# Performance work log

Measured on AMD Instinct MI355X. Metric: run time of the kernel, lower is better.

## Reference

```python
import jax, jax.numpy as jnp
import numpy as np

B, C, H, W = 8, 112, 64, 64
O, K, G = 112, 3, 14
STRIDE, PAD = 1, 1
K2 = K * K


def setup_inputs() -> dict:
    key = jax.random.key(0)
    ks = jax.random.split(key, 5)
    return {
        "x": jax.random.normal(ks[0], (B, C, H, W), jnp.float32),
        # offset/mask generator conv (3x3, stride 1, pad 1) -> 3*G*K2 channels
        "pg_weight": jax.random.normal(ks[1], (3 * G * K2, C, 3, 3), jnp.float32) * 0.01,
        "pg_bias": jax.random.normal(ks[2], (3 * G * K2,), jnp.float32) * 0.01,
        # main deformable-conv weight [O, C/groups, K, K] (groups=1) and bias
        "weight": jax.random.normal(ks[3], (O, C, K, K), jnp.float32) * 0.05,
        "bias": jax.random.normal(ks[4], (O,), jnp.float32) * 0.01,
    }


def _bilinear_sample(img, y, x):
    # img: [Cg, H, W]; y, x: [K2, Ho, Wo] float sampling coords.
    # Out-of-bounds corners contribute zero (torchvision semantics).
    Hi, Wi = img.shape[1], img.shape[2]
    y0 = jnp.floor(y)
    x0 = jnp.floor(x)

    def corner(yy, xx):
        valid = (yy >= 0) & (yy <= Hi - 1) & (xx >= 0) & (xx <= Wi - 1)
        yc = jnp.clip(yy, 0, Hi - 1).astype(jnp.int32)
        xc = jnp.clip(xx, 0, Wi - 1).astype(jnp.int32)
        v = img[:, yc, xc]  # [Cg, K2, Ho, Wo]
        return jnp.where(valid[None], v, jnp.zeros((), img.dtype))

    wy1 = (y - y0)[None]
    wx1 = (x - x0)[None]
    wy0 = 1.0 - wy1
    wx0 = 1.0 - wx1
    return (corner(y0, x0) * wy0 * wx0
            + corner(y0, x0 + 1) * wy0 * wx1
            + corner(y0 + 1, x0) * wy1 * wx0
            + corner(y0 + 1, x0 + 1) * wy1 * wx1)


def reference(x, pg_weight, pg_bias, weight, bias):
    Bn, Cn, Hn, Wn = x.shape
    Ho = (Hn + 2 * PAD - K) // STRIDE + 1
    Wo = (Wn + 2 * PAD - K) // STRIDE + 1
    # param_generator: 3x3 conv, stride 1, pad 1
    pg = jax.lax.conv_general_dilated(
        x, pg_weight, (1, 1), ((1, 1), (1, 1)),
        dimension_numbers=("NCHW", "OIHW", "NCHW"))
    pg = pg + pg_bias[None, :, None, None]
    GK2 = G * K2
    oh, ow, m = pg[:, :GK2], pg[:, GK2:2 * GK2], pg[:, 2 * GK2:]
    # module concatenates [oh, ow]; deform_conv2d interprets channels as [G, K2, (dy, dx)]
    off = jnp.concatenate([oh, ow], axis=1).reshape(Bn, G, K2, 2, Ho, Wo)
    dy, dx = off[:, :, :, 0], off[:, :, :, 1]
    mask = jax.nn.sigmoid(m).reshape(Bn, G, K2, Ho, Wo)
    # base sampling grid per kernel tap (row-major K*K order)
    ky = (jnp.arange(K2) // K).astype(x.dtype)
    kx = (jnp.arange(K2) % K).astype(x.dtype)
    py = (jnp.arange(Ho, dtype=x.dtype) * STRIDE - PAD)[None, :, None] + ky[:, None, None]
    px = (jnp.arange(Wo, dtype=x.dtype) * STRIDE - PAD)[None, None, :] + kx[:, None, None]
    ys = py[None, None] + dy  # [B, G, K2, Ho, Wo]
    xs = px[None, None] + dx
    xg = x.reshape(Bn, G, Cn // G, Hn, Wn)
    # vmap over batch, then offset group
    sampled = jax.vmap(jax.vmap(_bilinear_sample))(xg, ys, xs)  # [B, G, Cg, K2, Ho, Wo]
    sampled = sampled * mask[:, :, None]
    sampled = sampled.reshape(Bn, Cn, K2, Ho, Wo)
    out = jnp.einsum("bckhw,ock->bohw", sampled, weight.reshape(weight.shape[0], Cn, K2))
    return out + bias[None, :, None, None]
```

## Files before the change

kernel.cpp:

```cpp
#include <hip/hip_runtime.h>
#include <math.h>

#define Bn 8
#define Cn 112
#define Hn 64
#define Wn 64
#define On 112
#define Gn 14
#define PGC 378
#define HW 4096
#define CKW 1008
#define KP 1024
#define NP 384
#define XROW 4356
#define PG_MT 137
#define MPAD (PG_MT * 256)
#define PLANE_ROWS 34848
#define XGUARD 67
#define XTG_ROWS_TOTAL 558080

typedef __attribute__((ext_vector_type(8))) short bf16x8;
typedef __attribute__((ext_vector_type(4))) float f32x4;

__device__ __forceinline__ unsigned short f2bf(float f) {
    union { float f; unsigned int u; } v; v.f = f;
    unsigned int r = v.u + 0x7fffu + ((v.u >> 16) & 1u);
    return (unsigned short)(r >> 16);
}
__device__ __forceinline__ float bf2f(unsigned short u) {
    union { unsigned int u; float f; } v; v.u = ((unsigned int)u) << 16;
    return v.f;
}
__device__ __forceinline__ float bflo(unsigned int u) {
    union { unsigned int u; float f; } v; v.u = u << 16; return v.f;
}
__device__ __forceinline__ float bfhi(unsigned int u) {
    union { unsigned int u; float f; } v; v.u = u & 0xffff0000u; return v.f;
}
__device__ __forceinline__ void gload_lds16(const void* g, void* l) {
    __builtin_amdgcn_global_load_lds(
        (const __attribute__((address_space(1))) unsigned int*)g,
        (__attribute__((address_space(3))) unsigned int*)l, 16, 0, 0);
}

#define ZN XTG_ROWS_TOTAL
#define B2N (NP * KP)
#define WBN (128 * KP)
__global__ __launch_bounds__(256) void prep_kernel(
    const float* __restrict__ pgw, const float* __restrict__ w,
    unsigned short* __restrict__ XTGa, unsigned short* __restrict__ B2,
    unsigned short* __restrict__ WB)
{
    int t = blockIdx.x * 256 + threadIdx.x;
    if (t < ZN) {
        const uint4 z = {0, 0, 0, 0};
        reinterpret_cast<uint4*>(XTGa)[t] = z;
        return;
    }
    t -= ZN;
    if (t < B2N) {
        int oc = t >> 10, ck = t & 1023;
        int pg_ = ck >> 3, cc = ck & 7;
        int tap = pg_ / 14, pl = pg_ % 14;
        float v = (pg_ < 126 && oc < PGC)
            ? pgw[(size_t)oc * CKW + (pl * 8 + cc) * 9 + tap] : 0.f;
        B2[t] = f2bf(v);
        return;
    }
    t -= B2N;
    if (t < WBN) {
        int oc = t >> 10, ck = t & 1023;
        float v = 0.f;
        if (oc < On && ck < CKW) {
            int g = ck / 72, r = ck % 72;
            int k = r >> 3, cc = r & 7;
            v = w[(size_t)oc * CKW + (g * 8 + cc) * 9 + k];
        }
        WB[t] = f2bf(v);
    }
}

__global__ __launch_bounds__(256) void xpose_kernel(
    const float* __restrict__ x, unsigned short* __restrict__ XTG)
{
    __shared__ unsigned short lds[64][136];

    const int tid = threadIdx.x;
    const int y = blockIdx.x, b = blockIdx.y;
    const int xx = tid & 63, cw = tid >> 6;

    const float* xb = x + (size_t)b * Cn * HW + y * 64;
    #pragma unroll
    for (int p = 0; p < 28; ++p) {
        int c = p * 4 + cw;
        lds[xx][c] = f2bf(xb[(size_t)c * HW + xx]);
    }
    __syncthreads();

    #pragma unroll
    for (int q = 0; q < 4; ++q) {
        int task = q * 256 + tid;
        if (task < 896) {
            int g = task >> 6;
            int x2 = task & 63;
            unsigned short* dst = XTG + ((size_t)g * PLANE_ROWS
                + (size_t)b * XROW + (y + 1) * 66 + x2 + 1) * 8;
            *reinterpret_cast<uint4*>(dst) =
                *reinterpret_cast<const uint4*>(&lds[x2][g * 8]);
        }
    }
}

#define A_BUF_B 16384
#define B_BUF_B 8192
__global__ __launch_bounds__(512, 4) void pg_shift_kernel(
    const unsigned short* __restrict__ XTG, const unsigned short* __restrict__ B2,
    const float* __restrict__ pgb, unsigned short* __restrict__ pgBF)
{
    __shared__ __align__(16) unsigned char smem[3 * (A_BUF_B + B_BUF_B)];

    const int tid  = threadIdx.x;
    const int lane = tid & 63;
    const int w    = tid >> 6;
    const int wr   = w >> 1;
    const int wc   = w & 1;
    const int m0   = blockIdx.x * 256;
    const int n0   = blockIdx.y * 128;
    const int fr   = lane & 15, fq = lane >> 4;

    f32x4 acc[4][4] = {};

    auto Abuf = [&](int b) -> unsigned char* { return smem + b * A_BUF_B; };
    auto Bbuf = [&](int b) -> unsigned char* {
        return smem + 3 * A_BUF_B + b * B_BUF_B; };

    auto stage = [&](int buf, int kt) {
        #pragma unroll
        for (int s = 0; s < 2; ++s) {
            int r = w * 32 + s * 16 + (lane >> 2);
            int ch = (lane & 3) ^ ((r >> 1) & 3);
            int pg_ = kt * 4 + ch;
            int tap = pg_ / 14, pl = pg_ % 14;
            int shift = (tap / 3 - 1) * 66 + (tap % 3) - 1;
            if (pg_ >= 126) { pl = 14; shift = 0; }
            gload_lds16(XTG + ((long)pl * PLANE_ROWS + (long)(m0 + r) + shift) * 8,
                        Abuf(buf) + (w * 32 + s * 16) * 64);
        }
        {
            int r = w * 16 + (lane >> 2);
            int ch = (lane & 3) ^ ((r >> 1) & 3);
            gload_lds16(&B2[(size_t)(n0 + r) * KP + kt * 32 + ch * 8],
                        Bbuf(buf) + (w * 16) * 64);
        }
    };

    stage(0, 0);
    stage(1, 1);

    for (int kt = 0; kt < 32; ++kt) {
        if (kt < 31) asm volatile("s_waitcnt vmcnt(3)" ::: "memory");
        else         asm volatile("s_waitcnt vmcnt(0)" ::: "memory");
        __builtin_amdgcn_s_barrier();
        asm volatile("" ::: "memory");

        const int cur = kt % 3;
        const unsigned char* Ab = Abuf(cur);
        const unsigned char* Bb = Bbuf(cur);

        bf16x8 a[4], b[4];
        #pragma unroll
        for (int mi = 0; mi < 4; ++mi) {
            int r = wr * 64 + mi * 16 + fr;
            a[mi] = *reinterpret_cast<const bf16x8*>(
                Ab + r * 64 + ((fq ^ ((r >> 1) & 3)) << 4));
        }
        #pragma unroll
        for (int ni = 0; ni < 4; ++ni) {
            int r = wc * 64 + ni * 16 + fr;
            b[ni] = *reinterpret_cast<const bf16x8*>(
                Bb + r * 64 + ((fq ^ ((r >> 1) & 3)) << 4));
        }
        if (kt + 2 < 32) stage((kt + 2) % 3, kt + 2);

        __builtin_amdgcn_s_setprio(1);
        #pragma unroll
        for (int mi = 0; mi < 4; ++mi)
            #pragma unroll
            for (int ni = 0; ni < 4; ++ni)
                acc[mi][ni] = __builtin_amdgcn_mfma_f32_16x16x32_bf16(
                    a[mi], b[ni], acc[mi][ni], 0, 0, 0);
        __builtin_amdgcn_s_setprio(0);
    }

    __builtin_amdgcn_s_barrier();
    unsigned short* T = (unsigned short*)smem;

    #pragma unroll
    for (int ni = 0; ni < 4; ++ni) {
        int ocl = wc * 64 + ni * 16 + fr;
        float bv = (n0 + ocl < PGC) ? pgb[n0 + ocl] : 0.f;
        #pragma unroll
        for (int mi = 0; mi < 4; ++mi) {
            int pxl = wr * 64 + mi * 16 + fq * 4;
            ushort4 pk;
            pk.x = f2bf(acc[mi][ni][0] + bv);
            pk.y = f2bf(acc[mi][ni][1] + bv);
            pk.z = f2bf(acc[mi][ni][2] + bv);
            pk.w = f2bf(acc[mi][ni][3] + bv);
            *reinterpret_cast<ushort4*>(&T[ocl * 264 + pxl]) = pk;
        }
    }
    __builtin_amdgcn_s_barrier();

    const int pxls = tid & 255;
    const int half = tid >> 8;
    const int pxd  = m0 + pxls;
    const int bb   = pxd / XROW;
    const int rem  = pxd - bb * XROW;
    const int yy   = rem / 66 - 1;
    const int xx   = rem - (yy + 1) * 66 - 1;
    const bool valid = (pxd < Bn * XROW) &&
                       ((unsigned)yy < 64u) && ((unsigned)xx < 64u);
    unsigned short* pbase = pgBF + (size_t)bb * PGC * HW + yy * 64 + xx;

    #pragma unroll 4
    for (int oc = 0; oc < 64; ++oc) {
        int ocg = n0 + half * 64 + oc;
        if (ocg >= PGC) break;
        unsigned short v = T[(half * 64 + oc) * 264 + pxls];
        if (valid) pbase[(size_t)ocg * HW] = v;
    }
}

__global__ __launch_bounds__(512, 4) void fused_kernel(
    const unsigned short* __restrict__ XTG, const unsigned short* __restrict__ pg,
    const unsigned short* __restrict__ WB, const float* __restrict__ bias,
    float* __restrict__ out)
{
    __shared__ __align__(16) unsigned char Ab[2][64 * 128];
    __shared__ __align__(16) unsigned char Bb[2][128 * 128];

    const int tid  = threadIdx.x;
    const int lane = tid & 63;
    const int w    = tid >> 6;
    const int fr   = lane & 15, fq = lane >> 4;
    const int mh   = w >> 2;
    const int nq   = w & 3;

    const int bid = (int)blockIdx.x;
    const int blk = (bid & 7) * 64 + (bid >> 3);
    const int px0 = blk * 64;
    const int b   = px0 >> 12;
    const int hw0 = px0 & 4095;

    const int spx = lane;
    const int q   = w;
    const int hw  = hw0 + spx;
    const int sy  = hw >> 6, sx = hw & 63;

    const unsigned short* pgb = pg + (size_t)b * PGC * HW + hw;

    f32x4 acc[2][2] = {};

    unsigned short rdy, rdx, rmv;
    float fdy, fdx, fmv;
    uint4 q00, q01, q10, q11;
    float w00, w01, w10, w11;

    auto issue_pg = [&](int kt) {
        int gk = kt * 8 + q;
        int gkc = min(gk, 125);
        int g = gkc / 9, k = gkc - 9 * g;
        rdy = pgb[(size_t)(18 * g + 2 * k) * HW];
        rdx = pgb[(size_t)(18 * g + 2 * k + 1) * HW];
        rmv = pgb[(size_t)(252 + 9 * g + k) * HW];
    };

    auto issue_gather = [&](int kt1) {
        int gk = kt1 * 8 + q;
        bool valid = gk < 126;
        int gkc = min(gk, 125);
        int g = gkc / 9, k = gkc - 9 * g;
        const int ky = k / 3, kx = k - 3 * ky;
        float m = valid ? 1.f / (1.f + __expf(-fmv)) : 0.f;
        float yf = (float)(sy + ky - 1) + fdy;
        float xf = (float)(sx + kx - 1) + fdx;
        float y0 = floorf(yf), x0 = floorf(xf);
        float wy1 = yf - y0, wx1 = xf - x0;
        float wy0 = 1.f - wy1, wx0 = 1.f - wx1;
        int iy0 = (int)y0, ix0 = (int)x0;
        bool vy0 = (iy0 >= 0) && (iy0 < Hn);
        bool vy1 = (iy0 >= -1) && (iy0 < Hn - 1);
        bool vx0 = (ix0 >= 0) && (ix0 < Wn);
        bool vx1 = (ix0 >= -1) && (ix0 < Wn - 1);
        int cy0 = min(max(iy0, 0), Hn - 1), cy1 = min(max(iy0 + 1, 0), Hn - 1);
        int cx0 = min(max(ix0, 0), Wn - 1), cx1 = min(max(ix0 + 1, 0), Wn - 1);
        w00 = (vy0 && vx0) ? wy0 * wx0 * m : 0.f;
        w01 = (vy0 && vx1) ? wy0 * wx1 * m : 0.f;
        w10 = (vy1 && vx0) ? wy1 * wx0 * m : 0.f;
        w11 = (vy1 && vx1) ? wy1 * wx1 * m : 0.f;
        const unsigned short* xg = XTG +
            ((size_t)g * PLANE_ROWS + (size_t)b * XROW) * 8;
        q00 = *reinterpret_cast<const uint4*>(xg + (size_t)((cy0 + 1) * 66 + cx0 + 1) * 8);
        q01 = *reinterpret_cast<const uint4*>(xg + (size_t)((cy0 + 1) * 66 + cx1 + 1) * 8);
        q10 = *reinterpret_cast<const uint4*>(xg + (size_t)((cy1 + 1) * 66 + cx0 + 1) * 8);
        q11 = *reinterpret_cast<const uint4*>(xg + (size_t)((cy1 + 1) * 66 + cx1 + 1) * 8);
    };

    auto combine_write = [&](int buf) {
        unsigned int c00[4] = {q00.x, q00.y, q00.z, q00.w};
        unsigned int c01[4] = {q01.x, q01.y, q01.z, q01.w};
        unsigned int c10[4] = {q10.x, q10.y, q10.z, q10.w};
        unsigned int c11[4] = {q11.x, q11.y, q11.z, q11.w};
        unsigned int pk[4];
        #pragma unroll
        for (int j = 0; j < 4; ++j) {
            float lo = bflo(c00[j]) * w00 + bflo(c01[j]) * w01 +
                       bflo(c10[j]) * w10 + bflo(c11[j]) * w11;
            float hi = bfhi(c00[j]) * w00 + bfhi(c01[j]) * w01 +
                       bfhi(c10[j]) * w10 + bfhi(c11[j]) * w11;
            pk[j] = (unsigned int)f2bf(lo) | ((unsigned int)f2bf(hi) << 16);
        }
        int slot = q ^ (spx & 7);
        *reinterpret_cast<uint4*>(Ab[buf] + spx * 128 + slot * 16) =
            *reinterpret_cast<const uint4*>(pk);
    };

    auto stageB = [&](int buf, int kt) {
        #pragma unroll
        for (int s = 0; s < 2; ++s) {
            int r = s * 64 + w * 8 + (lane >> 3);
            int ch = (lane & 7) ^ (r & 7);
            gload_lds16(&WB[(size_t)r * KP + kt * 64 + ch * 8],
                        Bb[buf] + (s * 64 + w * 8) * 128);
        }
    };

    auto mfma_tile = [&](int c) {
        #pragma unroll
        for (int ks = 0; ks < 2; ++ks) {
            bf16x8 a[2], bfr[2];
            #pragma unroll
            for (int mi = 0; mi < 2; ++mi) {
                int r = mh * 32 + mi * 16 + fr;
                a[mi] = *reinterpret_cast<const bf16x8*>(
                    Ab[c] + r * 128 + (((ks * 4 + fq) ^ (r & 7)) << 4));
            }
            #pragma unroll
            for (int ni = 0; ni < 2; ++ni) {
                int r = nq * 32 + ni * 16 + fr;
                bfr[ni] = *reinterpret_cast<const bf16x8*>(
                    Bb[c] + r * 128 + (((ks * 4 + fq) ^ (r & 7)) << 4));
            }
            __builtin_amdgcn_s_setprio(1);
            #pragma unroll
            for (int mi = 0; mi < 2; ++mi)
                #pragma unroll
                for (int ni = 0; ni < 2; ++ni)
                    acc[mi][ni] = __builtin_amdgcn_mfma_f32_16x16x32_bf16(
                        a[mi], bfr[ni], acc[mi][ni], 0, 0, 0);
            __builtin_amdgcn_s_setprio(0);
        }
    };

    issue_pg(0);
    asm volatile("s_waitcnt vmcnt(0)" ::: "memory");
    fdy = bf2f(rdy); fdx = bf2f(rdx); fmv = bf2f(rmv);
    issue_gather(0);
    asm volatile("" ::: "memory");
    stageB(0, 0);
    asm volatile("" ::: "memory");
    issue_pg(1);
    asm volatile("s_waitcnt vmcnt(5)" ::: "memory");
    combine_write(0);
    asm volatile("s_waitcnt vmcnt(0)" ::: "memory");
    fdy = bf2f(rdy); fdx = bf2f(rdx); fmv = bf2f(rmv);
    asm volatile("s_waitcnt lgkmcnt(0)" ::: "memory");
    __builtin_amdgcn_s_barrier();
    asm volatile("" ::: "memory");

    int cur = 0;
    for (int kt = 0; kt < 16; ++kt) {
        if (kt < 15) {
            issue_gather(kt + 1);
            asm volatile("" ::: "memory");
            stageB(cur ^ 1, kt + 1);
            asm volatile("" ::: "memory");
            issue_pg(min(kt + 2, 15));
            asm volatile("" ::: "memory");
        }
        mfma_tile(cur);
        if (kt < 15) {
            asm volatile("s_waitcnt vmcnt(5)" ::: "memory");
            combine_write(cur ^ 1);
            asm volatile("s_waitcnt vmcnt(0)" ::: "memory");
            fdy = bf2f(rdy); fdx = bf2f(rdx); fmv = bf2f(rmv);
            asm volatile("s_waitcnt lgkmcnt(0)" ::: "memory");
            __builtin_amdgcn_s_barrier();
            asm volatile("" ::: "memory");
            cur ^= 1;
        }
    }

    #pragma unroll
    for (int ni = 0; ni < 2; ++ni) {
        int oc = nq * 32 + ni * 16 + fr;
        if (oc >= On) continue;
        float bv = bias[oc];
        #pragma unroll
        for (int mi = 0; mi < 2; ++mi) {
            int hwo = hw0 + mh * 32 + mi * 16 + fq * 4;
            float4 o;
            o.x = acc[mi][ni][0] + bv;
            o.y = acc[mi][ni][1] + bv;
            o.z = acc[mi][ni][2] + bv;
            o.w = acc[mi][ni][3] + bv;
            *reinterpret_cast<float4*>(
                &out[((size_t)(b * On + oc)) * HW + hwo]) = o;
        }
    }
}

extern "C" void kernel_launch(void* const* d_in, const int* in_sizes, int n_in,
                              void* d_out, int out_size, void* d_ws, size_t ws_size,
                              hipStream_t stream) {
    const float* x    = (const float*)d_in[0];
    const float* pgw  = (const float*)d_in[1];
    const float* pgb  = (const float*)d_in[2];
    const float* w    = (const float*)d_in[3];
    const float* bias = (const float*)d_in[4];
    float* out = (float*)d_out;

    char* wsb = (char*)d_ws;
    unsigned short* pgBF = (unsigned short*)wsb;
    size_t off = (size_t)PGC * Bn * HW * 2;
    unsigned short* B2   = (unsigned short*)(wsb + off);
    off += (size_t)NP * KP * 2;
    unsigned short* WB   = (unsigned short*)(wsb + off);
    off += (size_t)128 * KP * 2;
    unsigned short* XTGa = (unsigned short*)(wsb + off);
    unsigned short* XTG  = XTGa + (size_t)XGUARD * 8;

    {
        int tot = ZN + B2N + WBN;
        prep_kernel<<<(tot + 255) / 256, 256, 0, stream>>>(pgw, w, XTGa, B2, WB);
    }
    xpose_kernel<<<dim3(Hn, Bn), 256, 0, stream>>>(x, XTG);

    pg_shift_kernel<<<dim3(PG_MT, NP / 128), 512, 0, stream>>>(
        XTG, B2, pgb, pgBF);

    fused_kernel<<<dim3(512), 512, 0, stream>>>(XTG, pgBF, WB, bias, out);
}
```

Measured before the change: 91.75 us.

## Load shifted-input A fragments directly from global into registers, skipping LDS staging

In the offset-generator implicit GEMM, the A operand (shifted channel-last input planes) is now read straight from global memory into register fragments, double-buffered across iterations, instead of being staged through a triple-buffered LDS ring. Only the weight B tiles still go through LDS. This shrinks shared memory per block, which may allow higher occupancy, and removes LDS write/read traffic for A. The cost is that each wave issues its own uncoalesced-ish global loads, A data is no longer shared between the two column waves, and load latency has to be hidden by register prefetch one tile ahead.

New measurement: 88.01 us. -4.1%, faster.

```diff
diff --git a/kernel.cpp b/kernel.cpp
--- a/kernel.cpp
+++ b/kernel.cpp
@@ -111,13 +111,12 @@
     }
 }
 
-#define A_BUF_B 16384
 #define B_BUF_B 8192
 __global__ __launch_bounds__(512, 4) void pg_shift_kernel(
     const unsigned short* __restrict__ XTG, const unsigned short* __restrict__ B2,
     const float* __restrict__ pgb, unsigned short* __restrict__ pgBF)
 {
-    __shared__ __align__(16) unsigned char smem[3 * (A_BUF_B + B_BUF_B)];
+    __shared__ __align__(16) unsigned char smem[128 * 264 * 2];
 
     const int tid  = threadIdx.x;
     const int lane = tid & 63;
@@ -129,70 +128,73 @@
     const int fr   = lane & 15, fq = lane >> 4;
 
     f32x4 acc[4][4] = {};
-
-    auto Abuf = [&](int b) -> unsigned char* { return smem + b * A_BUF_B; };
-    auto Bbuf = [&](int b) -> unsigned char* {
-        return smem + 3 * A_BUF_B + b * B_BUF_B; };
-
-    auto stage = [&](int buf, int kt) {
-        #pragma unroll
-        for (int s = 0; s < 2; ++s) {
-            int r = w * 32 + s * 16 + (lane >> 2);
-            int ch = (lane & 3) ^ ((r >> 1) & 3);
-            int pg_ = kt * 4 + ch;
-            int tap = pg_ / 14, pl = pg_ % 14;
-            int shift = (tap / 3 - 1) * 66 + (tap % 3) - 1;
-            if (pg_ >= 126) { pl = 14; shift = 0; }
-            gload_lds16(XTG + ((long)pl * PLANE_ROWS + (long)(m0 + r) + shift) * 8,
-                        Abuf(buf) + (w * 32 + s * 16) * 64);
-        }
-        {
-            int r = w * 16 + (lane >> 2);
-            int ch = (lane & 3) ^ ((r >> 1) & 3);
-            gload_lds16(&B2[(size_t)(n0 + r) * KP + kt * 32 + ch * 8],
-                        Bbuf(buf) + (w * 16) * 64);
-        }
-    };
-
-    stage(0, 0);
-    stage(1, 1);
-
-    for (int kt = 0; kt < 32; ++kt) {
-        if (kt < 31) asm volatile("s_waitcnt vmcnt(3)" ::: "memory");
-        else         asm volatile("s_waitcnt vmcnt(0)" ::: "memory");
-        __builtin_amdgcn_s_barrier();
+    bf16x8 aFA[4], aFB[4];
+
+    auto Bbuf = [&](int b) -> unsigned char* { return smem + b * B_BUF_B; };
+
+    auto stageB = [&](int buf, int kt) {
+        int r = w * 16 + (lane >> 2);
+        int ch = (lane & 3) ^ ((r >> 1) & 3);
+        gload_lds16(&B2[(size_t)(n0 + r) * KP + kt * 32 + ch * 8],
+                    Bbuf(buf) + (w * 16) * 64);
+    };
+
+    auto loadA = [&](int kt, bf16x8 (&dst)[4]) {
+        int pg_ = kt * 4 + fq;
+        int tap = pg_ / 14, pl = pg_ % 14;
+        int shift = (tap / 3 - 1) * 66 + (tap % 3) - 1;
+        if (pg_ >= 126) { pl = 14; shift = 0; }
+        const unsigned short* base = XTG +
+            ((long)pl * PLANE_ROWS + (long)(m0 + shift)) * 8;
+        #pragma unroll
+        for (int mi = 0; mi < 4; ++mi) {
+            long r = wr * 64 + mi * 16 + fr;
+            dst[mi] = *reinterpret_cast<const bf16x8*>(base + r * 8);
+        }
+    };
+
+    auto tile_body = [&](int kt, bf16x8 (&aUse)[4], bf16x8 (&aNext)[4]) {
+        if (kt + 1 < 32) loadA(kt + 1, aNext);
         asm volatile("" ::: "memory");
-
-        const int cur = kt % 3;
-        const unsigned char* Ab = Abuf(cur);
-        const unsigned char* Bb = Bbuf(cur);
-
-        bf16x8 a[4], b[4];
-        #pragma unroll
-        for (int mi = 0; mi < 4; ++mi) {
-            int r = wr * 64 + mi * 16 + fr;
-            a[mi] = *reinterpret_cast<const bf16x8*>(
-                Ab + r * 64 + ((fq ^ ((r >> 1) & 3)) << 4));
-        }
+        if (kt + 2 < 32) stageB((kt + 2) % 3, kt + 2);
+        asm volatile("" ::: "memory");
+
+        const unsigned char* Bb = Bbuf(kt % 3);
+        bf16x8 b[4];
         #pragma unroll
         for (int ni = 0; ni < 4; ++ni) {
             int r = wc * 64 + ni * 16 + fr;
             b[ni] = *reinterpret_cast<const bf16x8*>(
                 Bb + r * 64 + ((fq ^ ((r >> 1) & 3)) << 4));
         }
-        if (kt + 2 < 32) stage((kt + 2) % 3, kt + 2);
-
         __builtin_amdgcn_s_setprio(1);
         #pragma unroll
         for (int mi = 0; mi < 4; ++mi)
             #pragma unroll
             for (int ni = 0; ni < 4; ++ni)
                 acc[mi][ni] = __builtin_amdgcn_mfma_f32_16x16x32_bf16(
-                    a[mi], b[ni], acc[mi][ni], 0, 0, 0);
+                    aUse[mi], b[ni], acc[mi][ni], 0, 0, 0);
         __builtin_amdgcn_s_setprio(0);
-    }
-
+
+        if (kt + 2 < 32) asm volatile("s_waitcnt vmcnt(1)" ::: "memory");
+        else             asm volatile("s_waitcnt vmcnt(0)" ::: "memory");
+        asm volatile("s_waitcnt lgkmcnt(0)" ::: "memory");
+        __builtin_amdgcn_s_barrier();
+        asm volatile("" ::: "memory");
+    };
+
+    stageB(0, 0);
+    stageB(1, 1);
+    loadA(0, aFA);
+    asm volatile("s_waitcnt vmcnt(0)" ::: "memory");
     __builtin_amdgcn_s_barrier();
+    asm volatile("" ::: "memory");
+
+    for (int kt = 0; kt < 32; kt += 2) {
+        tile_body(kt,     aFA, aFB);
+        tile_body(kt + 1, aFB, aFA);
+    }
+
     unsigned short* T = (unsigned short*)smem;
 
     #pragma unroll
```
